# Performance work log

Hardware: AMD Instinct MI355X
Metric: run time of the kernel (lower is better)

## Reference

```python
import jax, jax.numpy as jnp
import numpy as np

D = 4096  # input_dim
H = 4096  # hidden_dim


def setup_inputs() -> dict:
    key = jax.random.key(0)
    k_x, k_w, k_b, k_v, k_c = jax.random.split(key, 5)
    x = jax.random.uniform(k_x, (D, 1), dtype=jnp.float32)  # observed pixel values
    w = jax.random.normal(k_w, (H, D), dtype=jnp.float32) * 0.02
    b = jax.random.normal(k_b, (D, 1), dtype=jnp.float32) * 0.02
    v = jax.random.normal(k_v, (D, H), dtype=jnp.float32) * 0.02
    c = jax.random.normal(k_c, (H, 1), dtype=jnp.float32) * 0.02
    return {"x": x, "w": w, "b": b, "v": v, "c": c}


def reference(x, w, b, v, c):
    # Original loop: a_0 = c; a_{i+1} = a_i + w[:, i] * x[i]
    # => a_i = c + sum_{j < i} w[:, j] * x[j]  (exclusive cumsum of rank-1 updates)
    wx = w * x[:, 0][None, :]                      # [H, D]
    cum = jnp.cumsum(wx, axis=1)                   # inclusive cumsum over columns
    A = c + jnp.pad(cum[:, :-1], ((0, 0), (1, 0)))  # exclusive cumsum -> a_i in column i, [H, D]
    h = jax.nn.sigmoid(A)                          # h_i = sigmoid(a_i), [H, D]
    # p_i = sigmoid(v[i, :] @ h_i + b[i])
    logits = jnp.einsum("ih,hi->i", v, h)[:, None] + b  # [D, 1]
    p_x = jax.nn.sigmoid(logits)                   # [D, 1]
    return p_x
```

## Files before the change

kernel.cpp:

```cpp
#include <hip/hip_runtime.h>
#include <hip/hip_fp16.h>

#define D_DIM 4096
#define H_DIM 4096

__device__ __forceinline__ float fast_sigmoid(float a) {
    return __builtin_amdgcn_rcpf(1.0f + __expf(-a));
}

__global__ __launch_bounds__(256, 8) void nade_scan_kernel(
    const float* __restrict__ x,
    const float* __restrict__ w,
    const float* __restrict__ c,
    __half* __restrict__ S)
{
    __shared__ float qtot[4];

    const int tid  = threadIdx.x;
    const int q    = tid >> 6;
    const int lane = tid & 63;
    const int h    = blockIdx.x;
    const int col0 = q * 1024 + 8 * lane;

    const float* wp = w + (size_t)h * D_DIM + col0;
    const float* xp = x + col0;

    float4 w00 = *reinterpret_cast<const float4*>(wp);
    float4 w01 = *reinterpret_cast<const float4*>(wp + 4);
    float4 w10 = *reinterpret_cast<const float4*>(wp + 512);
    float4 w11 = *reinterpret_cast<const float4*>(wp + 512 + 4);
    float4 x00 = *reinterpret_cast<const float4*>(xp);
    float4 x01 = *reinterpret_cast<const float4*>(xp + 4);
    float4 x10 = *reinterpret_cast<const float4*>(xp + 512);
    float4 x11 = *reinterpret_cast<const float4*>(xp + 512 + 4);

    float l[16];
    float carry = 0.0f;

    #pragma unroll
    for (int t = 0; t < 2; ++t) {
        const float4 wv0 = t ? w10 : w00;
        const float4 wv1 = t ? w11 : w01;
        const float4 xv0 = t ? x10 : x00;
        const float4 xv1 = t ? x11 : x01;
        float p0 = wv0.x * xv0.x, p1 = wv0.y * xv0.y, p2 = wv0.z * xv0.z, p3 = wv0.w * xv0.w;
        float p4 = wv1.x * xv1.x, p5 = wv1.y * xv1.y, p6 = wv1.z * xv1.z, p7 = wv1.w * xv1.w;
        float s8 = ((p0 + p1) + (p2 + p3)) + ((p4 + p5) + (p6 + p7));
        float incl = s8;
        #pragma unroll
        for (int off = 1; off < 64; off <<= 1) {
            float tv = __shfl_up(incl, off, 64);
            incl += (lane >= off) ? tv : 0.0f;
        }
        float a = carry + incl - s8;
        l[8*t+0] = a; a += p0;
        l[8*t+1] = a; a += p1;
        l[8*t+2] = a; a += p2;
        l[8*t+3] = a; a += p3;
        l[8*t+4] = a; a += p4;
        l[8*t+5] = a; a += p5;
        l[8*t+6] = a; a += p6;
        l[8*t+7] = a;
        carry += __shfl(incl, 63, 64);
    }

    if (lane == 63) qtot[q] = carry;
    __syncthreads();

    float base = c[h];
    if (q >= 1) base += qtot[0];
    if (q >= 2) base += qtot[1];
    if (q >= 3) base += qtot[2];

    __half* sp = S + (size_t)h * D_DIM + col0;
    #pragma unroll
    for (int t = 0; t < 2; ++t) {
        union { __half2 h2[4]; uint4 u; } P;
        #pragma unroll
        for (int j = 0; j < 4; ++j)
            P.h2[j] = __floats2half2_rn(fast_sigmoid(l[8*t+2*j]   + base),
                                        fast_sigmoid(l[8*t+2*j+1] + base));
        *reinterpret_cast<uint4*>(sp + t * 512) = P.u;
    }
}

__global__ __launch_bounds__(256, 8) void nade_vdot_kernel(
    const float* __restrict__ v,
    const __half* __restrict__ S,
    float* __restrict__ part)
{
    __shared__ __half Sl[128][64];
    __shared__ float red[4][64];

    const int tid = threadIdx.x;
    const int it  = blockIdx.x & 63;
    const int ht  = blockIdx.x >> 6;
    const int i0  = it * 64;
    const int h0  = ht * 128;

    {
        const int r  = tid >> 3;
        const int c8 = tid & 7;
        #pragma unroll
        for (int p = 0; p < 4; ++p) {
            const int hh = p * 32 + r;
            uint4 d = *reinterpret_cast<const uint4*>(
                S + (size_t)(h0 + hh) * D_DIM + i0 + c8 * 8);
            *reinterpret_cast<uint4*>(&Sl[hh][c8 * 8]) = d;
        }
    }
    __syncthreads();

    const int il = tid & 63;
    const int q  = tid >> 6;
    const float* vp = v + (size_t)(i0 + il) * H_DIM + h0 + q * 32;

    float4 va[8];
    #pragma unroll
    for (int k = 0; k < 8; ++k)
        va[k] = *reinterpret_cast<const float4*>(vp + 4 * k);

    float acc = 0.0f;
    #pragma unroll
    for (int k = 0; k < 8; ++k) {
        const int hb = q * 32 + 4 * k;
        acc += va[k].x * __half2float(Sl[hb + 0][il])
             + va[k].y * __half2float(Sl[hb + 1][il])
             + va[k].z * __half2float(Sl[hb + 2][il])
             + va[k].w * __half2float(Sl[hb + 3][il]);
    }
    red[q][il] = acc;
    __syncthreads();
    if (q == 0)
        part[(size_t)ht * D_DIM + i0 + il] =
            red[0][il] + red[1][il] + red[2][il] + red[3][il];
}

__global__ __launch_bounds__(256, 8) void nade_out_kernel(
    const float* __restrict__ part,
    const float* __restrict__ b,
    float* __restrict__ out)
{
    const int i = blockIdx.x * 256 + threadIdx.x;
    float t = b[i];
    #pragma unroll
    for (int s = 0; s < 32; ++s)
        t += part[(size_t)s * D_DIM + i];
    out[i] = fast_sigmoid(t);
}

__global__ __launch_bounds__(1024, 1) void nade_fused_atomic(
    const float* __restrict__ x,
    const float* __restrict__ w,
    const float* __restrict__ v,
    const float* __restrict__ c,
    float* __restrict__ logits)
{
    __shared__ __half S[16][D_DIM];

    const int tid  = threadIdx.x;
    const int wv   = tid >> 6;
    const int lane = tid & 63;
    const int h0   = blockIdx.x * 16;

    const float* wrow = w + (size_t)(h0 + wv) * D_DIM + 8 * lane;
    float carry = c[h0 + wv];
    #pragma unroll
    for (int t = 0; t < 8; ++t) {
        float4 w0 = *reinterpret_cast<const float4*>(wrow + t * 512);
        float4 w1 = *reinterpret_cast<const float4*>(wrow + t * 512 + 4);
        float4 x0 = *reinterpret_cast<const float4*>(x + t * 512 + 8 * lane);
        float4 x1 = *reinterpret_cast<const float4*>(x + t * 512 + 8 * lane + 4);
        float p0 = w0.x * x0.x, p1 = w0.y * x0.y, p2 = w0.z * x0.z, p3 = w0.w * x0.w;
        float p4 = w1.x * x1.x, p5 = w1.y * x1.y, p6 = w1.z * x1.z, p7 = w1.w * x1.w;
        float s8 = ((p0 + p1) + (p2 + p3)) + ((p4 + p5) + (p6 + p7));
        float incl = s8;
        #pragma unroll
        for (int off = 1; off < 64; off <<= 1) {
            float tv = __shfl_up(incl, off, 64);
            incl += (lane >= off) ? tv : 0.0f;
        }
        float tot = __shfl(incl, 63, 64);
        float a = carry + incl - s8;
        float sg0 = fast_sigmoid(a); a += p0;
        float sg1 = fast_sigmoid(a); a += p1;
        float sg2 = fast_sigmoid(a); a += p2;
        float sg3 = fast_sigmoid(a); a += p3;
        float sg4 = fast_sigmoid(a); a += p4;
        float sg5 = fast_sigmoid(a); a += p5;
        float sg6 = fast_sigmoid(a); a += p6;
        float sg7 = fast_sigmoid(a);
        carry += tot;
        union { __half2 h2[4]; uint4 u; } P;
        P.h2[0] = __floats2half2_rn(sg0, sg1);
        P.h2[1] = __floats2half2_rn(sg2, sg3);
        P.h2[2] = __floats2half2_rn(sg4, sg5);
        P.h2[3] = __floats2half2_rn(sg6, sg7);
        *reinterpret_cast<uint4*>(&S[wv][t * 512 + 8 * lane]) = P.u;
    }
    __syncthreads();

    const int i0 = 4 * tid;
    float acc[4] = {0.f, 0.f, 0.f, 0.f};
    #pragma unroll
    for (int r = 0; r < 4; ++r) {
        const float* vp = v + (size_t)(i0 + r) * H_DIM + h0;
        float4 q0 = *reinterpret_cast<const float4*>(vp);
        float4 q1 = *reinterpret_cast<const float4*>(vp + 4);
        float4 q2 = *reinterpret_cast<const float4*>(vp + 8);
        float4 q3 = *reinterpret_cast<const float4*>(vp + 12);
        acc[r] = q0.x * __half2float(S[0][i0 + r])  + q0.y * __half2float(S[1][i0 + r])
               + q0.z * __half2float(S[2][i0 + r])  + q0.w * __half2float(S[3][i0 + r])
               + q1.x * __half2float(S[4][i0 + r])  + q1.y * __half2float(S[5][i0 + r])
               + q1.z * __half2float(S[6][i0 + r])  + q1.w * __half2float(S[7][i0 + r])
               + q2.x * __half2float(S[8][i0 + r])  + q2.y * __half2float(S[9][i0 + r])
               + q2.z * __half2float(S[10][i0 + r]) + q2.w * __half2float(S[11][i0 + r])
               + q3.x * __half2float(S[12][i0 + r]) + q3.y * __half2float(S[13][i0 + r])
               + q3.z * __half2float(S[14][i0 + r]) + q3.w * __half2float(S[15][i0 + r]);
    }
    #pragma unroll
    for (int r = 0; r < 4; ++r) atomicAdd(&logits[i0 + r], acc[r]);
}

__global__ __launch_bounds__(256, 1) void nade_final_atomic(
    const float* __restrict__ logits,
    const float* __restrict__ b,
    float* __restrict__ out)
{
    const int i = blockIdx.x * 256 + threadIdx.x;
    out[i] = fast_sigmoid(logits[i] + b[i]);
}

extern "C" void kernel_launch(void* const* d_in, const int* in_sizes, int n_in,
                              void* d_out, int out_size, void* d_ws, size_t ws_size,
                              hipStream_t stream)
{
    const float* x = (const float*)d_in[0];
    const float* w = (const float*)d_in[1];
    const float* b = (const float*)d_in[2];
    const float* v = (const float*)d_in[3];
    const float* c = (const float*)d_in[4];
    float* out = (float*)d_out;

    const size_t s_bytes    = (size_t)H_DIM * D_DIM * sizeof(__half);
    const size_t part_bytes = (size_t)32 * D_DIM * sizeof(float);

    if (ws_size >= s_bytes + part_bytes) {
        __half* S    = (__half*)d_ws;
        float*  part = (float*)((char*)d_ws + s_bytes);
        nade_scan_kernel<<<H_DIM, 256, 0, stream>>>(x, w, c, S);
        nade_vdot_kernel<<<64 * 32, 256, 0, stream>>>(v, S, part);
        nade_out_kernel<<<D_DIM / 256, 256, 0, stream>>>(part, b, out);
    } else {
        float* logits = (float*)d_ws;
        hipMemsetAsync(logits, 0, D_DIM * sizeof(float), stream);
        nade_fused_atomic<<<H_DIM / 16, 1024, 0, stream>>>(x, w, v, c, logits);
        nade_final_atomic<<<D_DIM / 256, 256, 0, stream>>>(logits, b, out);
    }
}
```

Baseline: 44.64 us.

## Coalesce v loads in vdot kernel with swizzled LDS and shuffle reduction

Reassigns threads in the v·S dot kernel so each half-wavefront reads a contiguous 128-float segment of one v row (coalesced) instead of each thread striding across rows. The S tile in shared memory is XOR-swizzled to avoid bank conflicts under the new access pattern, and the cross-thread sum now uses wave shuffles instead of a shared-memory reduction with a second barrier. The v loads are also issued before the barrier so they overlap the S tile fill. In exchange, every output needs a five-step shuffle reduction, which adds per-output instructions.

```diff
diff --git a/kernel.cpp b/kernel.cpp
--- a/kernel.cpp
+++ b/kernel.cpp
@@ -89,14 +89,15 @@
     const __half* __restrict__ S,
     float* __restrict__ part)
 {
-    __shared__ __half Sl[128][64];
-    __shared__ float red[4][64];
-
-    const int tid = threadIdx.x;
-    const int it  = blockIdx.x & 63;
-    const int ht  = blockIdx.x >> 6;
-    const int i0  = it * 64;
-    const int h0  = ht * 128;
+    __shared__ __half Sl[128 * 64];
+
+    const int tid  = threadIdx.x;
+    const int it   = blockIdx.x & 63;
+    const int ht   = blockIdx.x >> 6;
+    const int i0   = it * 64;
+    const int h0   = ht * 128;
+    const int lane = tid & 63;
+    const int wv   = tid >> 6;
 
     {
         const int r  = tid >> 3;
@@ -106,34 +107,41 @@
             const int hh = p * 32 + r;
             uint4 d = *reinterpret_cast<const uint4*>(
                 S + (size_t)(h0 + hh) * D_DIM + i0 + c8 * 8);
-            *reinterpret_cast<uint4*>(&Sl[hh][c8 * 8]) = d;
+            *reinterpret_cast<uint4*>(
+                &Sl[hh * 64 + ((c8 ^ ((hh >> 2) & 7)) << 3)]) = d;
         }
     }
+
+    const int hl  = (lane & 31) * 4;
+    const int rwb = wv * 16 + (lane >> 5);
+    float4 vr[8];
+    #pragma unroll
+    for (int j = 0; j < 8; ++j) {
+        const int row = rwb + 2 * j;
+        vr[j] = *reinterpret_cast<const float4*>(
+            v + (size_t)(i0 + row) * H_DIM + h0 + hl);
+    }
+
     __syncthreads();
 
-    const int il = tid & 63;
-    const int q  = tid >> 6;
-    const float* vp = v + (size_t)(i0 + il) * H_DIM + h0 + q * 32;
-
-    float4 va[8];
-    #pragma unroll
-    for (int k = 0; k < 8; ++k)
-        va[k] = *reinterpret_cast<const float4*>(vp + 4 * k);
-
-    float acc = 0.0f;
-    #pragma unroll
-    for (int k = 0; k < 8; ++k) {
-        const int hb = q * 32 + 4 * k;
-        acc += va[k].x * __half2float(Sl[hb + 0][il])
-             + va[k].y * __half2float(Sl[hb + 1][il])
-             + va[k].z * __half2float(Sl[hb + 2][il])
-             + va[k].w * __half2float(Sl[hb + 3][il]);
-    }
-    red[q][il] = acc;
-    __syncthreads();
-    if (q == 0)
-        part[(size_t)ht * D_DIM + i0 + il] =
-            red[0][il] + red[1][il] + red[2][il] + red[3][il];
+    auto sget = [&](int h_loc, int i) -> float {
+        return __half2float(
+            Sl[h_loc * 64 + ((((i) >> 3) ^ ((h_loc >> 2) & 7)) << 3) + (i & 7)]);
+    };
+
+    #pragma unroll
+    for (int j = 0; j < 8; ++j) {
+        const int row = rwb + 2 * j;
+        float acc = vr[j].x * sget(hl + 0, row)
+                  + vr[j].y * sget(hl + 1, row)
+                  + vr[j].z * sget(hl + 2, row)
+                  + vr[j].w * sget(hl + 3, row);
+        #pragma unroll
+        for (int mask = 1; mask <= 16; mask <<= 1)
+            acc += __shfl_xor(acc, mask, 64);
+        if ((lane & 31) == 0)
+            part[(size_t)ht * D_DIM + i0 + row] = acc;
+    }
 }
 
 __global__ __launch_bounds__(256, 8) void nade_out_kernel(
```

Measured after the change: 43.73 us. 1.02x faster.
